# Kernel optimization log

Measured on AMD Instinct MI355X. Metric: run time of the kernel, lower is better.

Reference implementation:

```python
import jax, jax.numpy as jnp
import numpy as np
from jax import lax

STRIDE = 4
RADII = [0.1, 0.2, 0.4, 0.8]   # initial radius 0.1, radius_scaling=2 per stage
NSAMPLE = 32
# per-stage conv channels [c_in(+3 for dp), c1, c2, c3]
CH = [[6, 64, 64, 128], [131, 128, 128, 256], [259, 256, 256, 512], [515, 512, 512, 1024]]


def _fps(xyz, npoint):
    """Furthest point sampling: xyz [B,N,3] -> idx [B,npoint] int32 (indices, no grad)."""
    xyz = lax.stop_gradient(xyz)
    B, N, _ = xyz.shape
    first = jnp.zeros((B,), jnp.int32)

    def step(carry, _):
        dists, last = carry
        lp = jnp.take_along_axis(xyz, last[:, None, None], axis=1)   # [B,1,3]
        d = jnp.sum((xyz - lp) ** 2, axis=-1)                        # [B,N]
        dists = jnp.minimum(dists, d)
        nxt = jnp.argmax(dists, axis=-1).astype(jnp.int32)
        return (dists, nxt), nxt

    init = (jnp.full((B, N), 1e10, xyz.dtype), first)
    _, rest = lax.scan(step, init, None, length=npoint - 1)          # [npoint-1, B]
    return jnp.concatenate([first[None], rest], axis=0).T            # [B, npoint]


def _ball_query(query, support, radius, nsample):
    """First nsample in-radius neighbor indices (lowest index first), padded with the
    first hit -- same semantics as the PointNet++ CUDA ball_query kernel."""
    query = lax.stop_gradient(query)
    support = lax.stop_gradient(support)
    N = support.shape[1]
    d2 = jnp.sum((query[:, :, None, :] - support[:, None, :, :]) ** 2, axis=-1)  # [B,Q,N]
    ar = jnp.arange(N, dtype=jnp.int32)
    key = jnp.where(d2 < radius * radius, ar[None, None, :], N)     # in-radius -> own index, else N
    neg_vals, order = lax.top_k(-key, nsample)                      # smallest indices first
    valid = (-neg_vals) < N
    return jnp.where(valid, order, order[..., :1])                  # [B,Q,nsample]


def _gather_pts(pts, idx):   # pts [B,N,3], idx [B,Q,S] -> [B,Q,S,3]
    return jax.vmap(lambda p, i: p[i])(pts, idx)


def _gather_feat(f, idx):    # f [B,C,N], idx [B,Q,S] -> [B,C,Q,S]
    return jax.vmap(lambda fb, i: fb[:, i])(f, idx)


def _local_aggr(query_xyz, support_xyz, feats, Ws, bs, radius, nsample):
    idx = _ball_query(query_xyz, support_xyz, radius, nsample)
    dp = _gather_pts(support_xyz, idx) - query_xyz[:, :, None, :]    # [B,Q,S,3] relative coords
    f = jnp.concatenate([jnp.transpose(dp, (0, 3, 1, 2)),            # [B,3,Q,S]
                         _gather_feat(feats, idx)], axis=1)          # [B,3+C,Q,S]
    for W, b in zip(Ws, bs):                                         # pointwise MLP over neighbors
        f = jax.nn.relu(jnp.einsum('oc,bcqs->boqs', W, f) + b[None, :, None, None])
    return jnp.max(f, axis=-1)                                       # max-pool over neighborhood -> [B,C_out,Q]


def _forward(xyz, Ws, bs):
    feats = jnp.transpose(xyz, (0, 2, 1))                            # features default to xyz^T: [B,3,N]
    support = xyz
    for k in range(4):                                               # 4 SA stages, stride 4 each
        npoint = support.shape[1] // STRIDE
        idx = _fps(support, npoint)
        query = jnp.take_along_axis(support, idx[:, :, None], axis=1)  # [B,npoint,3]
        feats = _local_aggr(query, support, feats, Ws[k], bs[k], RADII[k], NSAMPLE)
        support = query
    return feats                                                     # [B,1024,64]


def setup_inputs() -> dict:
    key = jax.random.key(0)
    ks = jax.random.split(key, 32)
    inp = {"xyz": jax.random.uniform(ks[0], (2, 16384, 3), jnp.float32)}
    i = 1
    for k in range(4):
        for l in range(3):
            cin, cout = CH[k][l], CH[k][l + 1]
            inp[f"w{k}{l}"] = jax.random.normal(ks[i], (cout, cin), jnp.float32) / np.sqrt(cin).astype(np.float32)
            i += 1
            inp[f"b{k}{l}"] = 0.01 * jax.random.normal(ks[i], (cout,), jnp.float32)
            i += 1
    return inp


def reference(xyz, w00, b00, w01, b01, w02, b02,
              w10, b10, w11, b11, w12, b12,
              w20, b20, w21, b21, w22, b22,
              w30, b30, w31, b31, w32, b32):
    Ws = [[w00, w01, w02], [w10, w11, w12], [w20, w21, w22], [w30, w31, w32]]
    bs = [[b00, b01, b02], [b10, b11, b12], [b20, b21, b22], [b30, b31, b32]]
    return _forward(xyz, Ws, bs)
```

## Files before the change

kernel.cpp:

```cpp
#include <hip/hip_runtime.h>
#include <cstdint>
#include <cstddef>

#define NBATCH 2
#define NSAMPLE 32

__global__ void xyzT_kernel(const float* __restrict__ xyz, float* __restrict__ xyzT, int N)
{
    int t = blockIdx.x * blockDim.x + threadIdx.x;
    int total = NBATCH * N;
    if (t >= total) return;
    int b = t / N, n = t - b * N;
    const float* p = xyz + ((size_t)b * N + n) * 3;
    float* o = xyzT + (size_t)b * 3 * N + n;
    o[0]            = p[0];
    o[(size_t)N]    = p[1];
    o[2 * (size_t)N] = p[2];
}

template<int PPT, int BT, int MINW>
__global__ __launch_bounds__(BT, MINW)
void fps_kernel(const float* __restrict__ xyz, int npoint,
                float* __restrict__ query)
{
    const int N = PPT * BT;
    constexpr int NW = BT / 64;
    const int b = blockIdx.x;
    const int t = threadIdx.x;
    const int lane = t & 63;
    const int wid  = t >> 6;
    const float* xb = xyz + (size_t)b * N * 3;

    float px[PPT], py[PPT], pz[PPT], dd[PPT];
#pragma unroll
    for (int i = 0; i < PPT; ++i) {
        int p = i * BT + t;
        px[i] = xb[p * 3 + 0];
        py[i] = xb[p * 3 + 1];
        pz[i] = xb[p * 3 + 2];
        dd[i] = 1e10f;
    }

    __shared__ unsigned long long s_wkey[2][NW];

    float cx = xb[0], cy = xb[1], cz = xb[2];
    if (t == 0) {
        float* q = query + (size_t)b * npoint * 3;
        q[0] = cx; q[1] = cy; q[2] = cz;
    }

    for (int step = 1; step < npoint; ++step) {
        const int buf = step & 1;
        float bd = -1.0f;
        int bslot = 0;
#pragma unroll
        for (int i = 0; i < PPT; ++i) {
            float dx = px[i] - cx, dy = py[i] - cy, dz = pz[i] - cz;
            float d = __fmul_rn(dx, dx);
            d = __fadd_rn(d, __fmul_rn(dy, dy));
            d = __fadd_rn(d, __fmul_rn(dz, dz));
            float nd = fminf(dd[i], d);
            dd[i] = nd;
            bool g = nd > bd;
            bd    = g ? nd : bd;
            bslot = g ? i : bslot;
        }
        int bidx = bslot * BT + t;
        unsigned long long key =
            ((unsigned long long)__float_as_uint(bd) << 32) | (unsigned int)(~bidx);
#pragma unroll
        for (int m = 1; m < 64; m <<= 1) {
            unsigned long long o = __shfl_xor(key, m);
            key = (o > key) ? o : key;
        }
        if (lane == 0) s_wkey[buf][wid] = key;
        __syncthreads();
        unsigned long long v[NW];
#pragma unroll
        for (int w = 0; w < NW; ++w) v[w] = s_wkey[buf][w];
#pragma unroll
        for (int s = NW / 2; s > 0; s >>= 1)
#pragma unroll
            for (int w = 0; w < NW / 2; ++w)
                if (w < s) v[w] = (v[w + s] > v[w]) ? v[w + s] : v[w];
        unsigned int widx = ~(unsigned int)v[0];
        const float* wp = xb + (size_t)widx * 3;
        cx = wp[0]; cy = wp[1]; cz = wp[2];
        if (t == 0) {
            float* q = query + ((size_t)b * npoint + step) * 3;
            q[0] = cx; q[1] = cy; q[2] = cz;
        }
    }
}

__global__ void ballquery_kernel(const float* __restrict__ support,
                                 const float* __restrict__ query,
                                 int N, int Q, float r2,
                                 int* __restrict__ nbr)
{
    int gw   = (blockIdx.x * blockDim.x + threadIdx.x) >> 6;
    int lane = threadIdx.x & 63;
    if (gw >= NBATCH * Q) return;
    int b = gw / Q;
    int q = gw - b * Q;

    const float* sb = support + (size_t)b * N * 3;
    const float* qp = query + ((size_t)b * Q + q) * 3;
    float qx = qp[0], qy = qp[1], qz = qp[2];
    int* out = nbr + ((size_t)b * Q + q) * NSAMPLE;

    int cnt = 0, first = 0;
    for (int base = 0; base < N; base += 64) {
        int j = base + lane;
        float dx = __fsub_rn(sb[j * 3 + 0], qx);
        float dy = __fsub_rn(sb[j * 3 + 1], qy);
        float dz = __fsub_rn(sb[j * 3 + 2], qz);
        float d2 = __fmul_rn(dx, dx);
        d2 = __fadd_rn(d2, __fmul_rn(dy, dy));
        d2 = __fadd_rn(d2, __fmul_rn(dz, dz));
        bool inr = d2 < r2;
        unsigned long long mask = __ballot(inr);
        if (mask) {
            if (cnt == 0) first = base + (int)__builtin_ctzll(mask);
            if (inr) {
                int pos = cnt + (int)__popcll(mask & ((1ull << lane) - 1ull));
                if (pos < NSAMPLE) out[pos] = j;
            }
            cnt += (int)__popcll(mask);
            if (cnt >= NSAMPLE) break;
        }
    }
    for (int pos = cnt + lane; pos < NSAMPLE; pos += 64) out[pos] = first;
}

__global__ void gather_kernel(const float* __restrict__ support,
                              const float* __restrict__ query,
                              const int* __restrict__ nbr,
                              const float* __restrict__ feats,
                              int N, int Q, int C, int b,
                              float* __restrict__ F0)
{
    int n = blockIdx.x * blockDim.x + threadIdx.x;
    int Nn = Q * NSAMPLE;
    if (n >= Nn) return;
    int q = n >> 5, s = n & 31;
    int j = nbr[((size_t)b * Q + q) * NSAMPLE + s];
    const float* sp = support + ((size_t)b * N + j) * 3;
    const float* qp = query + ((size_t)b * Q + q) * 3;
    size_t NnS = (size_t)Nn;
    F0[n]           = sp[0] - qp[0];
    F0[NnS + n]     = sp[1] - qp[1];
    F0[2 * NnS + n] = sp[2] - qp[2];
    const float* fb = feats + (size_t)b * C * N;
    float* Fo = F0 + 3 * NnS + n;
    for (int c = 0; c < C; ++c) Fo[(size_t)c * NnS] = fb[(size_t)c * N + j];
}

template<bool POOL>
__global__ __launch_bounds__(256)
void gemm_relu(const float* __restrict__ W, const float* __restrict__ bias,
               const float* __restrict__ F, float* __restrict__ Out,
               int M, int K, int Nn, int b)
{
    __shared__ float Ws[16][64];
    __shared__ float Fs[16][68];

    const int n0 = blockIdx.x * 64;
    const int m0 = blockIdx.y * 64;
    const int tid = threadIdx.x;
    const int tx = tid & 15, ty = tid >> 4;

    float acc[4][4] = {};

    const int wm = tid >> 2;
    const int wk = (tid & 3) * 4;
    const int fk = tid >> 4;
    const int fn = (tid & 15) * 4;

    for (int k0 = 0; k0 < K; k0 += 16) {
#pragma unroll
        for (int j = 0; j < 4; ++j) {
            int kk = wk + j;
            int kg = k0 + kk;
            Ws[kk][wm] = (kg < K) ? W[(size_t)(m0 + wm) * K + kg] : 0.0f;
        }
        {
            int kg = k0 + fk;
            float4 v = make_float4(0.f, 0.f, 0.f, 0.f);
            if (kg < K) v = *(const float4*)(F + (size_t)kg * Nn + n0 + fn);
            *(float4*)&Fs[fk][fn] = v;
        }
        __syncthreads();
#pragma unroll
        for (int kk = 0; kk < 16; ++kk) {
            float av[4], bv[4];
            *(float4*)av = *(const float4*)&Ws[kk][ty * 4];
            *(float4*)bv = *(const float4*)&Fs[kk][tx * 4];
#pragma unroll
            for (int i = 0; i < 4; ++i)
#pragma unroll
                for (int j = 0; j < 4; ++j)
                    acc[i][j] = fmaf(av[i], bv[j], acc[i][j]);
        }
        __syncthreads();
    }

    if constexpr (!POOL) {
#pragma unroll
        for (int i = 0; i < 4; ++i) {
            int m = m0 + ty * 4 + i;
            float bvs = bias[m];
            float4 r;
            r.x = fmaxf(acc[i][0] + bvs, 0.0f);
            r.y = fmaxf(acc[i][1] + bvs, 0.0f);
            r.z = fmaxf(acc[i][2] + bvs, 0.0f);
            r.w = fmaxf(acc[i][3] + bvs, 0.0f);
            *(float4*)(Out + (size_t)m * Nn + n0 + tx * 4) = r;
        }
    } else {
        __shared__ float Cs[64][65];
#pragma unroll
        for (int i = 0; i < 4; ++i) {
            int mr = ty * 4 + i;
            float bvs = bias[m0 + mr];
#pragma unroll
            for (int j = 0; j < 4; ++j)
                Cs[mr][tx * 4 + j] = fmaxf(acc[i][j] + bvs, 0.0f);
        }
        __syncthreads();
        if (tid < 128) {
            int r = tid >> 1, g = tid & 1;
            float mx = Cs[r][g * 32];
            for (int c = 1; c < 32; ++c) mx = fmaxf(mx, Cs[r][g * 32 + c]);
            int Qn = Nn >> 5;
            Out[((size_t)b * M + m0 + r) * Qn + (n0 >> 5) + g] = mx;
        }
    }
}

extern "C" void kernel_launch(void* const* d_in, const int* in_sizes, int n_in,
                              void* d_out, int out_size, void* d_ws, size_t ws_size,
                              hipStream_t stream)
{
    (void)in_sizes; (void)n_in; (void)out_size; (void)ws_size;
    const float* xyz = (const float*)d_in[0];
    const float* W[4][3]; const float* Bi[4][3];
    for (int k = 0; k < 4; ++k)
        for (int l = 0; l < 3; ++l) {
            W[k][l]  = (const float*)d_in[1 + k * 6 + l * 2];
            Bi[k][l] = (const float*)d_in[2 + k * 6 + l * 2];
        }
    float* out = (float*)d_out;

    uintptr_t cur = (uintptr_t)d_ws;
    auto alloc = [&](size_t bytes) -> void* {
        void* p = (void*)cur;
        cur += (bytes + 255) & ~(size_t)255;
        return p;
    };
    float* xyzT = (float*)alloc((size_t)NBATCH * 3 * 16384 * sizeof(float));
    float* qA   = (float*)alloc((size_t)NBATCH * 4096 * 3 * sizeof(float));
    float* qB   = (float*)alloc((size_t)NBATCH * 4096 * 3 * sizeof(float));
    int*   nbr  = (int*)  alloc((size_t)NBATCH * 4096 * NSAMPLE * sizeof(int));
    float* f0   = (float*)alloc((size_t)NBATCH * 128 * 4096 * sizeof(float));
    float* f1   = (float*)alloc((size_t)NBATCH * 256 * 1024 * sizeof(float));
    float* f2   = (float*)alloc((size_t)NBATCH * 512 * 256 * sizeof(float));
    float* X = (float*)alloc((size_t)8388608 * sizeof(float));
    float* Y = (float*)alloc((size_t)8388608 * sizeof(float));

    xyzT_kernel<<<(NBATCH * 16384 + 255) / 256, 256, 0, stream>>>(xyz, xyzT, 16384);

    struct StageP { int N, Q, Cprev, c1, c2, c3; double r; };
    const StageP st[4] = {
        {16384, 4096,   3,   64,  64,  128, 0.1},
        { 4096, 1024, 128,  128, 128,  256, 0.2},
        { 1024,  256, 256,  256, 256,  512, 0.4},
        {  256,   64, 512,  512, 512, 1024, 0.8},
    };
    const float* support   = xyz;
    const float* featsPrev = xyzT;
    float* qbuf[2]     = {qA, qB};
    float* featsOut[4] = {f0, f1, f2, out};

    for (int k = 0; k < 4; ++k) {
        const StageP& s = st[k];
        float* qcur = qbuf[k & 1];
        if      (k == 0) fps_kernel<32, 512, 2><<<NBATCH, 512, 0, stream>>>(support, s.Q, qcur);
        else if (k == 1) fps_kernel< 8, 512, 2><<<NBATCH, 512, 0, stream>>>(support, s.Q, qcur);
        else if (k == 2) fps_kernel< 2, 512, 2><<<NBATCH, 512, 0, stream>>>(support, s.Q, qcur);
        else             fps_kernel< 1, 256, 1><<<NBATCH, 256, 0, stream>>>(support, s.Q, qcur);

        float r2 = (float)(s.r * s.r);
        ballquery_kernel<<<(NBATCH * s.Q) / 4, 256, 0, stream>>>(support, qcur, s.N, s.Q, r2, nbr);

        int K0 = 3 + s.Cprev;
        int Nn = s.Q * NSAMPLE;
        for (int b = 0; b < NBATCH; ++b) {
            gather_kernel<<<(Nn + 255) / 256, 256, 0, stream>>>(
                support, qcur, nbr, featsPrev, s.N, s.Q, s.Cprev, b, X);
            gemm_relu<false><<<dim3(Nn / 64, s.c1 / 64, 1), 256, 0, stream>>>(
                W[k][0], Bi[k][0], X, Y, s.c1, K0, Nn, 0);
            gemm_relu<false><<<dim3(Nn / 64, s.c2 / 64, 1), 256, 0, stream>>>(
                W[k][1], Bi[k][1], Y, X, s.c2, s.c1, Nn, 0);
            gemm_relu<true><<<dim3(Nn / 64, s.c3 / 64, 1), 256, 0, stream>>>(
                W[k][2], Bi[k][2], X, featsOut[k], s.c3, s.c2, Nn, b);
        }
        support   = qcur;
        featsPrev = featsOut[k];
    }
}
```

Measured before the change: 9.333 ms.

## Move FPS point coordinates into shared memory and widen stage-0 block to 1024

Furthest point sampling kernels now keep point coordinates in LDS instead of per-thread registers. Stage 0 uses a dedicated 1024-thread kernel that stores x/y pairs in 128KB of shared memory, keeps only z and distances in registers, and reads two points per float4 load. Later stages store float4-padded points in LDS. This lowers register pressure and allows more threads per block for the serial FPS loop. In exchange, every iteration adds LDS reads and reduces across 16 waves instead of 8.

```diff
diff --git a/kernel.cpp b/kernel.cpp
--- a/kernel.cpp
+++ b/kernel.cpp
@@ -18,30 +18,33 @@
     o[2 * (size_t)N] = p[2];
 }
 
-template<int PPT, int BT, int MINW>
-__global__ __launch_bounds__(BT, MINW)
-void fps_kernel(const float* __restrict__ xyz, int npoint,
-                float* __restrict__ query)
-{
-    const int N = PPT * BT;
-    constexpr int NW = BT / 64;
+__global__ __launch_bounds__(1024)
+__attribute__((amdgpu_waves_per_eu(4, 4)))
+void fps_s0(const float* __restrict__ xyz, int npoint, float* __restrict__ query)
+{
+    const int N = 16384, BT = 1024;
+    const int NW = 16;
+    __shared__ float s_xy[2 * 16384];
+    __shared__ unsigned long long s_wkey[2][NW];
+
     const int b = blockIdx.x;
     const int t = threadIdx.x;
     const int lane = t & 63;
     const int wid  = t >> 6;
     const float* xb = xyz + (size_t)b * N * 3;
 
-    float px[PPT], py[PPT], pz[PPT], dd[PPT];
-#pragma unroll
-    for (int i = 0; i < PPT; ++i) {
-        int p = i * BT + t;
-        px[i] = xb[p * 3 + 0];
-        py[i] = xb[p * 3 + 1];
-        pz[i] = xb[p * 3 + 2];
-        dd[i] = 1e10f;
-    }
-
-    __shared__ unsigned long long s_wkey[2][NW];
+    float pz[16], dd[16];
+#pragma unroll
+    for (int i = 0; i < 8; ++i)
+#pragma unroll
+        for (int j = 0; j < 2; ++j) {
+            int p = 2 * (i * BT + t) + j;
+            const float* pp = xb + (size_t)p * 3;
+            s_xy[2 * p]     = pp[0];
+            s_xy[2 * p + 1] = pp[1];
+            pz[2 * i + j]   = pp[2];
+            dd[2 * i + j]   = 1e10f;
+        }
 
     float cx = xb[0], cy = xb[1], cz = xb[2];
     if (t == 0) {
@@ -54,8 +57,98 @@
         float bd = -1.0f;
         int bslot = 0;
 #pragma unroll
+        for (int i = 0; i < 8; ++i) {
+            const float4 v = *(const float4*)&s_xy[4 * (i * BT + t)];
+            {
+                float dx = v.x - cx, dy = v.y - cy, dz = pz[2 * i] - cz;
+                float d = __fmul_rn(dx, dx);
+                d = __fadd_rn(d, __fmul_rn(dy, dy));
+                d = __fadd_rn(d, __fmul_rn(dz, dz));
+                float nd = fminf(dd[2 * i], d);
+                dd[2 * i] = nd;
+                bool g = nd > bd;
+                bd    = g ? nd : bd;
+                bslot = g ? (2 * i) : bslot;
+            }
+            {
+                float dx = v.z - cx, dy = v.w - cy, dz = pz[2 * i + 1] - cz;
+                float d = __fmul_rn(dx, dx);
+                d = __fadd_rn(d, __fmul_rn(dy, dy));
+                d = __fadd_rn(d, __fmul_rn(dz, dz));
+                float nd = fminf(dd[2 * i + 1], d);
+                dd[2 * i + 1] = nd;
+                bool g = nd > bd;
+                bd    = g ? nd : bd;
+                bslot = g ? (2 * i + 1) : bslot;
+            }
+        }
+        int bidx = 2 * ((bslot >> 1) * BT + t) + (bslot & 1);
+        unsigned long long key =
+            ((unsigned long long)__float_as_uint(bd) << 32) | (unsigned int)(~bidx);
+#pragma unroll
+        for (int m = 1; m < 64; m <<= 1) {
+            unsigned long long o = __shfl_xor(key, m);
+            key = (o > key) ? o : key;
+        }
+        if (lane == 0) s_wkey[buf][wid] = key;
+        __syncthreads();
+        unsigned long long v[NW];
+#pragma unroll
+        for (int w = 0; w < NW; ++w) v[w] = s_wkey[buf][w];
+#pragma unroll
+        for (int s = NW / 2; s > 0; s >>= 1)
+#pragma unroll
+            for (int w = 0; w < NW / 2; ++w)
+                if (w < s) v[w] = (v[w + s] > v[w]) ? v[w + s] : v[w];
+        unsigned int widx = ~(unsigned int)v[0];
+        const float* wp = xb + (size_t)widx * 3;
+        cx = wp[0]; cy = wp[1]; cz = wp[2];
+        if (t == 0) {
+            float* q = query + ((size_t)b * npoint + step) * 3;
+            q[0] = cx; q[1] = cy; q[2] = cz;
+        }
+    }
+}
+
+template<int PPT, int BT, int WPE>
+__global__ __launch_bounds__(BT)
+__attribute__((amdgpu_waves_per_eu(WPE, WPE)))
+void fps_gen(const float* __restrict__ xyz, int npoint, float* __restrict__ query)
+{
+    const int N = PPT * BT;
+    constexpr int NW = BT / 64;
+    __shared__ float4 s_p[PPT * BT];
+    __shared__ unsigned long long s_wkey[2][NW];
+
+    const int b = blockIdx.x;
+    const int t = threadIdx.x;
+    const int lane = t & 63;
+    const int wid  = t >> 6;
+    const float* xb = xyz + (size_t)b * N * 3;
+
+    float dd[PPT];
+#pragma unroll
+    for (int i = 0; i < PPT; ++i) {
+        int p = i * BT + t;
+        const float* pp = xb + (size_t)p * 3;
+        s_p[p] = make_float4(pp[0], pp[1], pp[2], 0.0f);
+        dd[i] = 1e10f;
+    }
+
+    float cx = xb[0], cy = xb[1], cz = xb[2];
+    if (t == 0) {
+        float* q = query + (size_t)b * npoint * 3;
+        q[0] = cx; q[1] = cy; q[2] = cz;
+    }
+
+    for (int step = 1; step < npoint; ++step) {
+        const int buf = step & 1;
+        float bd = -1.0f;
+        int bslot = 0;
+#pragma unroll
         for (int i = 0; i < PPT; ++i) {
-            float dx = px[i] - cx, dy = py[i] - cy, dz = pz[i] - cz;
+            const float4 v = s_p[i * BT + t];
+            float dx = v.x - cx, dy = v.y - cy, dz = v.z - cz;
             float d = __fmul_rn(dx, dx);
             d = __fadd_rn(d, __fmul_rn(dy, dy));
             d = __fadd_rn(d, __fmul_rn(dz, dz));
@@ -285,10 +378,10 @@
     for (int k = 0; k < 4; ++k) {
         const StageP& s = st[k];
         float* qcur = qbuf[k & 1];
-        if      (k == 0) fps_kernel<32, 512, 2><<<NBATCH, 512, 0, stream>>>(support, s.Q, qcur);
-        else if (k == 1) fps_kernel< 8, 512, 2><<<NBATCH, 512, 0, stream>>>(support, s.Q, qcur);
-        else if (k == 2) fps_kernel< 2, 512, 2><<<NBATCH, 512, 0, stream>>>(support, s.Q, qcur);
-        else             fps_kernel< 1, 256, 1><<<NBATCH, 256, 0, stream>>>(support, s.Q, qcur);
+        if      (k == 0) fps_s0<<<NBATCH, 1024, 0, stream>>>(support, s.Q, qcur);
+        else if (k == 1) fps_gen<8, 512, 2><<<NBATCH, 512, 0, stream>>>(support, s.Q, qcur);
+        else if (k == 2) fps_gen<2, 512, 2><<<NBATCH, 512, 0, stream>>>(support, s.Q, qcur);
+        else             fps_gen<1, 256, 1><<<NBATCH, 256, 0, stream>>>(support, s.Q, qcur);
 
         float r2 = (float)(s.r * s.r);
         ballquery_kernel<<<(NBATCH * s.Q) / 4, 256, 0, stream>>>(support, qcur, s.N, s.Q, r2, nbr);
```

New measurement: 10.28 ms. 1.1x slower.
